# Performance work log

Hardware: AMD Instinct MI355X
Metric: run time of the kernel (lower is better)

Reference implementation:

```python
import jax, jax.numpy as jnp
import numpy as np

NEG = -1e30  # stands in for -inf on the diagonal; exp(NEG - max) == 0 exactly


def setup_inputs() -> dict:
    key = jax.random.key(0)
    k1, k2, k3, k4, k5 = jax.random.split(key, 5)
    B, C, H, W = 4, 512, 128, 128
    mid = C // 8  # 64
    x = jax.random.normal(k1, (B, C, H, W), dtype=jnp.float32)
    Wq = jax.random.normal(k2, (mid, C), dtype=jnp.float32) * (1.0 / np.sqrt(C))
    Wk = jax.random.normal(k3, (mid, C), dtype=jnp.float32) * (1.0 / np.sqrt(C))
    Wv = jax.random.normal(k4, (C, C), dtype=jnp.float32) * (1.0 / np.sqrt(C))
    gamma = jax.random.normal(k5, (1,), dtype=jnp.float32) * 0.1
    return {"x": x, "Wq": Wq, "Wk": Wk, "Wv": Wv, "gamma": gamma}


def reference(x, Wq, Wk, Wv, gamma):
    B, C, H, W = x.shape
    # 1x1 convs == channel matmuls
    q = jnp.einsum('bchw,mc->bmhw', x, Wq)  # (B, mid, H, W)
    k = jnp.einsum('bchw,mc->bmhw', x, Wk)
    v = jnp.einsum('bchw,dc->bdhw', x, Wv)  # (B, C, H, W)

    # vertical (H-axis) logits with -inf diagonal: eH[b,i,w,j] = sum_m q[b,m,i,w] k[b,m,j,w]
    eH = jnp.einsum('bmiw,bmjw->biwj', q, k)           # (B, H, W, H)
    diag = jnp.eye(H, dtype=bool)[:, None, :]          # (H, 1, H)
    eH = jnp.where(diag, NEG, eH)

    # horizontal (W-axis) logits: eW[b,h,i,j] = sum_m q[b,m,h,i] k[b,m,h,j]
    eW = jnp.einsum('bmhi,bmhj->bhij', q, k)           # (B, H, W, W)

    # joint softmax over the concatenated H+W logits
    attn = jax.nn.softmax(jnp.concatenate([eH, eW], axis=3), axis=3)  # (B, H, W, H+W)
    aH = attn[:, :, :, :H]  # (B, H, W, H)
    aW = attn[:, :, :, H:]  # (B, H, W, W)

    # attention-weighted value aggregation along each axis
    outH = jnp.einsum('bcjw,biwj->bciw', v, aH)  # (B, C, H, W)
    outW = jnp.einsum('bchj,bhij->bchi', v, aW)  # (B, C, H, W)

    return gamma[0] * (outH + outW) + x
```

## Files before the change

kernel.cpp:

```cpp
#include <hip/hip_runtime.h>
#include <cstdint>
#include <cstddef>

#define NEGV (-1e30f)

constexpr int C_ = 512, H_ = 128, W_ = 128;
constexpr int P_ = 16384;

typedef short bf16x8 __attribute__((ext_vector_type(8)));
typedef float f32x4  __attribute__((ext_vector_type(4)));
#define MFMA16(a, b, c) __builtin_amdgcn_mfma_f32_16x16x32_bf16((a), (b), (c), 0, 0, 0)

__device__ inline unsigned short f2bf(float f) {
    union { float f; uint32_t i; } t; t.f = f;
    uint32_t r = t.i + 0x7FFFu + ((t.i >> 16) & 1u);
    return (unsigned short)(r >> 16);
}
__device__ inline float bf2f(unsigned short u) {
    union { uint32_t i; float f; } t; t.i = (uint32_t)u << 16; return t.f;
}

__global__ __launch_bounds__(256) void kwconv(
    const float* __restrict__ Wq, const float* __restrict__ Wk,
    const float* __restrict__ Wv,
    unsigned short* __restrict__ Wqkbf, unsigned short* __restrict__ Wvbf)
{
    const int i4 = (blockIdx.x * 256 + threadIdx.x) * 4;
    const float* src; unsigned short* dst; int off;
    if (i4 < 32768)       { src = Wq + i4;          dst = Wqkbf + i4; }
    else if (i4 < 65536)  { off = i4 - 32768; src = Wk + off; dst = Wqkbf + i4; }
    else                  { off = i4 - 65536; src = Wv + off; dst = Wvbf + off; }
    const float4 v = *(const float4*)src;
    ushort4 u; u.x = f2bf(v.x); u.y = f2bf(v.y); u.z = f2bf(v.z); u.w = f2bf(v.w);
    *(ushort4*)dst = u;
}

__global__ __launch_bounds__(256) void kprep1(
    const float* __restrict__ x, unsigned short* __restrict__ xTbf)
{
    __shared__ float t[32][33];
    const int tx = threadIdx.x, ty = threadIdx.y;
    const int h0 = (blockIdx.x >> 2) * 32, w0 = (blockIdx.x & 3) * 32;
    const size_t base = (size_t)blockIdx.y * P_;
#pragma unroll
    for (int k = 0; k < 4; k++)
        t[ty + 8 * k][tx] = x[base + (size_t)(h0 + ty + 8 * k) * 128 + w0 + tx];
    __syncthreads();
#pragma unroll
    for (int k = 0; k < 4; k++)
        xTbf[base + (size_t)(w0 + ty + 8 * k) * 128 + h0 + tx] = f2bf(t[tx][ty + 8 * k]);
}

__global__ __launch_bounds__(256) void kprep2(
    const float* __restrict__ x, unsigned short* __restrict__ xbfT)
{
    __shared__ float t[32][33];
    const int tx = threadIdx.x, ty = threadIdx.y;
    const int p0 = blockIdx.x * 32, c0 = blockIdx.y * 32, b = blockIdx.z;
#pragma unroll
    for (int k = 0; k < 4; k++)
        t[ty + 8 * k][tx] = x[((size_t)(b * C_ + c0 + ty + 8 * k)) * P_ + p0 + tx];
    __syncthreads();
#pragma unroll
    for (int k = 0; k < 4; k++)
        xbfT[((size_t)b * P_ + p0 + ty + 8 * k) * C_ + c0 + tx] = f2bf(t[tx][ty + 8 * k]);
}

__global__ __launch_bounds__(256) void kgemm_mfma(
    const unsigned short* __restrict__ A, const unsigned short* __restrict__ Bm,
    unsigned short* __restrict__ outbf, float* __restrict__ outf,
    const float* __restrict__ addx, const float* __restrict__ gammap)
{
    __shared__ __attribute__((aligned(16))) unsigned short sA[128 * 72];
    __shared__ __attribute__((aligned(16))) unsigned short sB[128 * 72];
    const int tid = threadIdx.x;
    const int pbase = blockIdx.x * 128, mt = blockIdx.y, b = blockIdx.z;
    const int lane = tid & 63, wv = tid >> 6;
    const int m0 = (wv >> 1) * 64, p0 = (wv & 1) * 64;
    const int fr = lane & 15, fq = lane >> 4;

    f32x4 acc[4][4];
#pragma unroll
    for (int i = 0; i < 4; i++)
#pragma unroll
        for (int j = 0; j < 4; j++) acc[i][j] = (f32x4){0.f, 0.f, 0.f, 0.f};

    const size_t arow0 = (size_t)(mt * 128) * 512;
    const size_t brow0 = ((size_t)b * P_ + pbase) * 512;

    for (int kc = 0; kc < 512; kc += 64) {
#pragma unroll
        for (int rep = 0; rep < 4; rep++) {
            const int idx = rep * 256 + tid;
            const int kg = idx & 7, r = idx >> 3;
            *(uint4*)&sA[r * 72 + kg * 8] = *(const uint4*)&A[arow0 + (size_t)r * 512 + kc + kg * 8];
            *(uint4*)&sB[r * 72 + kg * 8] = *(const uint4*)&Bm[brow0 + (size_t)r * 512 + kc + kg * 8];
        }
        __syncthreads();
#pragma unroll
        for (int kk = 0; kk < 64; kk += 32) {
            bf16x8 af[4], bfv[4];
#pragma unroll
            for (int t = 0; t < 4; t++) af[t]  = *(const bf16x8*)&sA[(m0 + t * 16 + fr) * 72 + kk + fq * 8];
#pragma unroll
            for (int t = 0; t < 4; t++) bfv[t] = *(const bf16x8*)&sB[(p0 + t * 16 + fr) * 72 + kk + fq * 8];
#pragma unroll
            for (int i = 0; i < 4; i++)
#pragma unroll
                for (int j = 0; j < 4; j++)
                    acc[i][j] = MFMA16(af[i], bfv[j], acc[i][j]);
        }
        __syncthreads();
    }

    if (outbf) {
#pragma unroll
        for (int tj = 0; tj < 4; tj++) {
            const int p_g = pbase + p0 + tj * 16 + fr;
            const size_t rowo = ((size_t)b * P_ + p_g) * 128;
#pragma unroll
            for (int ti = 0; ti < 4; ti++) {
                const int mk = m0 + ti * 16 + fq * 4;
                ushort4 u;
                u.x = f2bf(acc[ti][tj][0]); u.y = f2bf(acc[ti][tj][1]);
                u.z = f2bf(acc[ti][tj][2]); u.w = f2bf(acc[ti][tj][3]);
                *(ushort4*)&outbf[rowo + mk] = u;
            }
        }
    } else {
        const float g = gammap[0];
#pragma unroll
        for (int ti = 0; ti < 4; ti++)
#pragma unroll
            for (int r = 0; r < 4; r++) {
                const int m_g = mt * 128 + m0 + ti * 16 + fq * 4 + r;
                const size_t rowo = ((size_t)(b * 512 + m_g)) * P_;
#pragma unroll
                for (int tj = 0; tj < 4; tj++) {
                    const int p_g = pbase + p0 + tj * 16 + fr;
                    outf[rowo + p_g] = fmaf(g, acc[ti][tj][r], addx[rowo + p_g]);
                }
            }
    }
}

__global__ __launch_bounds__(256) void klogits(
    const unsigned short* __restrict__ qkP, float* __restrict__ E,
    int rowMul, int rowStep, int mask)
{
    __shared__ __attribute__((aligned(16))) unsigned short sPM[128 * 136];
    const int tid = threadIdx.x;
    const int s = blockIdx.x, b = blockIdx.y;
    const size_t qbase = (size_t)b * P_ * 128;
    const int rb = s * rowMul;
#pragma unroll
    for (int rep = 0; rep < 8; rep++) {
        const int idx = rep * 256 + tid;
        const int mkg = idx & 15, i = idx >> 4;
        *(uint4*)&sPM[i * 136 + mkg * 8] =
            *(const uint4*)&qkP[qbase + (size_t)(rb + i * rowStep) * 128 + mkg * 8];
    }
    __syncthreads();

    const int lane = tid & 63, wv = tid >> 6;
    const int i0 = (wv >> 1) * 64, j0 = (wv & 1) * 64;
    const int fr = lane & 15, fq = lane >> 4;

    f32x4 acc[4][4];
#pragma unroll
    for (int i = 0; i < 4; i++)
#pragma unroll
        for (int j = 0; j < 4; j++) acc[i][j] = (f32x4){0.f, 0.f, 0.f, 0.f};

#pragma unroll
    for (int kk = 0; kk < 64; kk += 32) {
        bf16x8 af[4], bfv[4];
#pragma unroll
        for (int t = 0; t < 4; t++) af[t]  = *(const bf16x8*)&sPM[(i0 + t * 16 + fr) * 136 + kk + fq * 8];
#pragma unroll
        for (int t = 0; t < 4; t++) bfv[t] = *(const bf16x8*)&sPM[(j0 + t * 16 + fr) * 136 + 64 + kk + fq * 8];
#pragma unroll
        for (int i = 0; i < 4; i++)
#pragma unroll
            for (int j = 0; j < 4; j++)
                acc[i][j] = MFMA16(af[i], bfv[j], acc[i][j]);
    }

    float* Eb = E + ((size_t)(b * 128 + s)) * P_;
#pragma unroll
    for (int ti = 0; ti < 4; ti++)
#pragma unroll
        for (int r = 0; r < 4; r++) {
            const int i_g = i0 + ti * 16 + fq * 4 + r;
#pragma unroll
            for (int tj = 0; tj < 4; tj++) {
                const int j_g = j0 + tj * 16 + fr;
                float v = acc[ti][tj][r];
                if (mask && i_g == j_g) v = NEGV;
                Eb[(size_t)i_g * 128 + j_g] = v;
            }
        }
}

__global__ __launch_bounds__(256) void ksoftmax(
    const float* __restrict__ ER, const float* __restrict__ EC,
    unsigned short* __restrict__ AR, unsigned short* __restrict__ AC)
{
    const int lane = threadIdx.x & 63;
    const int pix = blockIdx.x * 4 + (threadIdx.x >> 6);
    const int b = pix >> 14, rem = pix & 16383;
    const int h = rem >> 7, w = rem & 127;
    const size_t ro = ((size_t)((b * 128 + h) * 128 + w)) * 128;
    const size_t co = ((size_t)((b * 128 + w) * 128 + h)) * 128;
    const float2 r = *(const float2*)(ER + ro + lane * 2);
    const float2 c = *(const float2*)(EC + co + lane * 2);
    float mx = fmaxf(fmaxf(r.x, r.y), fmaxf(c.x, c.y));
#pragma unroll
    for (int off = 32; off > 0; off >>= 1) mx = fmaxf(mx, __shfl_xor(mx, off));
    const float e0 = __expf(r.x - mx), e1 = __expf(r.y - mx);
    const float e2 = __expf(c.x - mx), e3 = __expf(c.y - mx);
    float sm = e0 + e1 + e2 + e3;
#pragma unroll
    for (int off = 32; off > 0; off >>= 1) sm += __shfl_xor(sm, off);
    const float inv = 1.0f / sm;
    ushort2 u0; u0.x = f2bf(e0 * inv); u0.y = f2bf(e1 * inv);
    ushort2 u1; u1.x = f2bf(e2 * inv); u1.y = f2bf(e3 * inv);
    *(ushort2*)(AR + ro + lane * 2) = u0;
    *(ushort2*)(AC + co + lane * 2) = u1;
}

__global__ __launch_bounds__(256) void kagg(
    const unsigned short* __restrict__ At, const float* __restrict__ Xf,
    const unsigned short* __restrict__ Xbf, unsigned short* __restrict__ ySumT,
    int pMul, int pStep, int rmw)
{
    __shared__ __attribute__((aligned(16))) unsigned short sA[128 * 72];
    __shared__ __attribute__((aligned(16))) unsigned short sB[128 * 72];
    const int tid = threadIdx.x;
    const int s = blockIdx.x, b = blockIdx.y, ct = blockIdx.z;
    const int lane = tid & 63, wv = tid >> 6;
    const int m0 = (wv >> 1) * 64, n0 = (wv & 1) * 64;
    const int fr = lane & 15, fq = lane >> 4;
    const size_t abase = ((size_t)(b * 128 + s)) * P_;

    f32x4 acc[4][4];
#pragma unroll
    for (int i = 0; i < 4; i++)
#pragma unroll
        for (int j = 0; j < 4; j++) acc[i][j] = (f32x4){0.f, 0.f, 0.f, 0.f};

    for (int kc = 0; kc < 128; kc += 64) {
#pragma unroll
        for (int rep = 0; rep < 4; rep++) {
            const int idx = rep * 256 + tid;
            const int jg = idx & 7, i = idx >> 3;
            *(uint4*)&sA[i * 72 + jg * 8] = *(const uint4*)&At[abase + (size_t)i * 128 + kc + jg * 8];
        }
        if (Xf) {
#pragma unroll
            for (int rep = 0; rep < 8; rep++) {
                const int idx = rep * 256 + tid;
                const int jq = idx & 15, cc = idx >> 4;
                const float4 v = *(const float4*)&Xf[((size_t)(b * C_ + ct * 128 + cc)) * P_ + s * 128 + kc + jq * 4];
                ushort4 u; u.x = f2bf(v.x); u.y = f2bf(v.y); u.z = f2bf(v.z); u.w = f2bf(v.w);
                *(ushort4*)&sB[cc * 72 + jq * 4] = u;
            }
        } else {
#pragma unroll
            for (int rep = 0; rep < 4; rep++) {
                const int idx = rep * 256 + tid;
                const int jg = idx & 7, cc = idx >> 3;
                *(uint4*)&sB[cc * 72 + jg * 8] =
                    *(const uint4*)&Xbf[((size_t)(b * C_ + ct * 128 + cc)) * P_ + s * 128 + kc + jg * 8];
            }
        }
        __syncthreads();
#pragma unroll
        for (int kk = 0; kk < 64; kk += 32) {
            bf16x8 af[4], bfv[4];
#pragma unroll
            for (int t = 0; t < 4; t++) af[t]  = *(const bf16x8*)&sA[(m0 + t * 16 + fr) * 72 + kk + fq * 8];
#pragma unroll
            for (int t = 0; t < 4; t++) bfv[t] = *(const bf16x8*)&sB[(n0 + t * 16 + fr) * 72 + kk + fq * 8];
#pragma unroll
            for (int i = 0; i < 4; i++)
#pragma unroll
                for (int j = 0; j < 4; j++)
                    acc[i][j] = MFMA16(af[i], bfv[j], acc[i][j]);
        }
        __syncthreads();
    }

#pragma unroll
    for (int ti = 0; ti < 4; ti++)
#pragma unroll
        for (int r = 0; r < 4; r++) {
            const int i_g = m0 + ti * 16 + fq * 4 + r;
            const size_t p = (size_t)s * pMul + (size_t)i_g * pStep;
            const size_t rowo = ((size_t)b * P_ + p) * 512;
#pragma unroll
            for (int tc = 0; tc < 4; tc++) {
                const int c_g = ct * 128 + n0 + tc * 16 + fr;
                float v = acc[ti][tc][r];
                if (rmw) v += bf2f(ySumT[rowo + c_g]);
                ySumT[rowo + c_g] = f2bf(v);
            }
        }
}

extern "C" void kernel_launch(void* const* d_in, const int* in_sizes, int n_in,
                              void* d_out, int out_size, void* d_ws, size_t ws_size,
                              hipStream_t stream) {
    const float* x     = (const float*)d_in[0];
    const float* Wq    = (const float*)d_in[1];
    const float* Wk    = (const float*)d_in[2];
    const float* Wv    = (const float*)d_in[3];
    const float* gamma = (const float*)d_in[4];
    float* out = (float*)d_out;

    char* base = (char*)d_ws;
    unsigned short* Wqkbf = (unsigned short*)base;             base += 131072;
    unsigned short* Wvbf  = (unsigned short*)base;             base += 524288;
    unsigned short* xTbf  = (unsigned short*)base;             base += 67108864;
    unsigned short* xbfT  = (unsigned short*)base;             base += 67108864;
    unsigned short* qkP   = (unsigned short*)base;             base += 16777216;
    float*          ERow  = (float*)base;                      base += 33554432;
    float*          ECol  = (float*)base;                      base += 33554432;
    unsigned short* ARow  = (unsigned short*)base;             base += 16777216;
    unsigned short* ACol  = (unsigned short*)base;             base += 16777216;
    unsigned short* ySumT = (unsigned short*)base;             base += 67108864;

    kwconv<<<320, 256, 0, stream>>>(Wq, Wk, Wv, Wqkbf, Wvbf);
    kprep1<<<dim3(16, 2048), dim3(32, 8), 0, stream>>>(x, xTbf);
    kprep2<<<dim3(512, 16, 4), dim3(32, 8), 0, stream>>>(x, xbfT);
    kgemm_mfma<<<dim3(128, 1, 4), 256, 0, stream>>>(Wqkbf, xbfT, qkP, nullptr, nullptr, nullptr);
    klogits<<<dim3(128, 4), 256, 0, stream>>>(qkP, ERow, 128, 1, 0);
    klogits<<<dim3(128, 4), 256, 0, stream>>>(qkP, ECol, 1, 128, 1);
    ksoftmax<<<16384, 256, 0, stream>>>(ERow, ECol, ARow, ACol);
    kagg<<<dim3(128, 4, 4), 256, 0, stream>>>(ARow, x, nullptr, ySumT, 128, 1, 0);
    kagg<<<dim3(128, 4, 4), 256, 0, stream>>>(ACol, nullptr, xTbf, ySumT, 1, 128, 1);
    kgemm_mfma<<<dim3(128, 4, 4), 256, 0, stream>>>(Wvbf, ySumT, nullptr, out, x, gamma);
}
```

Measured before the change: 553.8 us.

## Merge aggregation passes into one kernel with separate row/column sums and swizzled LDS

Replaces the two kagg launches, which read-modify-write a shared ySumT buffer, with one kagg2 launch. It writes row and column aggregates to separate buffers, the column one aliasing the no-longer-needed ERow, and loops over all four channel tiles while keeping the attention tile resident in swizzled LDS. The final value GEMM sums the two bf16 buffers while loading its B operand. The two logits launches are also merged via blockIdx.z. This removes the RMW read pass and the repeated attention loads, at the cost of extra bf16 adds and rounding in the final GEMM's load path and a larger LDS footprint per block.

New measurement: 558.4 us. No clear change (+0.8%).

```diff
diff --git a/kernel.cpp b/kernel.cpp
--- a/kernel.cpp
+++ b/kernel.cpp
@@ -10,6 +10,8 @@
 typedef short bf16x8 __attribute__((ext_vector_type(8)));
 typedef float f32x4  __attribute__((ext_vector_type(4)));
 #define MFMA16(a, b, c) __builtin_amdgcn_mfma_f32_16x16x32_bf16((a), (b), (c), 0, 0, 0)
+
+#define SWZI(r, cu) ((((r) << 7)) + (((((cu) >> 3) ^ ((r) & 15))) << 3) + ((cu) & 7))
 
 __device__ inline unsigned short f2bf(float f) {
     union { float f; uint32_t i; } t; t.f = f;
@@ -18,6 +20,17 @@
 }
 __device__ inline float bf2f(unsigned short u) {
     union { uint32_t i; float f; } t; t.i = (uint32_t)u << 16; return t.f;
+}
+__device__ inline uint32_t bfadd2(uint32_t a, uint32_t b) {
+    union { uint32_t i; float f; } alo, ahi, blo, bhi;
+    alo.i = a << 16; ahi.i = a & 0xffff0000u;
+    blo.i = b << 16; bhi.i = b & 0xffff0000u;
+    const float lo = alo.f + blo.f, hi = ahi.f + bhi.f;
+    return (uint32_t)f2bf(lo) | ((uint32_t)f2bf(hi) << 16);
+}
+__device__ inline uint4 bfadd8(const uint4 a, const uint4 b) {
+    uint4 r; r.x = bfadd2(a.x, b.x); r.y = bfadd2(a.y, b.y);
+    r.z = bfadd2(a.z, b.z); r.w = bfadd2(a.w, b.w); return r;
 }
 
 __global__ __launch_bounds__(256) void kwconv(
@@ -68,6 +81,7 @@
 
 __global__ __launch_bounds__(256) void kgemm_mfma(
     const unsigned short* __restrict__ A, const unsigned short* __restrict__ Bm,
+    const unsigned short* __restrict__ Bm2,
     unsigned short* __restrict__ outbf, float* __restrict__ outf,
     const float* __restrict__ addx, const float* __restrict__ gammap)
 {
@@ -94,7 +108,10 @@
             const int idx = rep * 256 + tid;
             const int kg = idx & 7, r = idx >> 3;
             *(uint4*)&sA[r * 72 + kg * 8] = *(const uint4*)&A[arow0 + (size_t)r * 512 + kc + kg * 8];
-            *(uint4*)&sB[r * 72 + kg * 8] = *(const uint4*)&Bm[brow0 + (size_t)r * 512 + kc + kg * 8];
+            const size_t boff = brow0 + (size_t)r * 512 + kc + kg * 8;
+            uint4 vb = *(const uint4*)&Bm[boff];
+            if (Bm2) vb = bfadd8(vb, *(const uint4*)&Bm2[boff]);
+            *(uint4*)&sB[r * 72 + kg * 8] = vb;
         }
         __syncthreads();
 #pragma unroll
@@ -145,12 +162,15 @@
 }
 
 __global__ __launch_bounds__(256) void klogits(
-    const unsigned short* __restrict__ qkP, float* __restrict__ E,
-    int rowMul, int rowStep, int mask)
+    const unsigned short* __restrict__ qkP,
+    float* __restrict__ ERow, float* __restrict__ ECol)
 {
     __shared__ __attribute__((aligned(16))) unsigned short sPM[128 * 136];
     const int tid = threadIdx.x;
-    const int s = blockIdx.x, b = blockIdx.y;
+    const int s = blockIdx.x, b = blockIdx.y, mode = blockIdx.z;
+    const int rowMul  = mode ? 1 : 128;
+    const int rowStep = mode ? 128 : 1;
+    float* E = mode ? ECol : ERow;
     const size_t qbase = (size_t)b * P_ * 128;
     const int rb = s * rowMul;
 #pragma unroll
@@ -196,7 +216,7 @@
             for (int tj = 0; tj < 4; tj++) {
                 const int j_g = j0 + tj * 16 + fr;
                 float v = acc[ti][tj][r];
-                if (mask && i_g == j_g) v = NEGV;
+                if (mode && i_g == j_g) v = NEGV;
                 Eb[(size_t)i_g * 128 + j_g] = v;
             }
         }
@@ -229,83 +249,86 @@
     *(ushort2*)(AC + co + lane * 2) = u1;
 }
 
-__global__ __launch_bounds__(256) void kagg(
-    const unsigned short* __restrict__ At, const float* __restrict__ Xf,
-    const unsigned short* __restrict__ Xbf, unsigned short* __restrict__ ySumT,
-    int pMul, int pStep, int rmw)
-{
-    __shared__ __attribute__((aligned(16))) unsigned short sA[128 * 72];
-    __shared__ __attribute__((aligned(16))) unsigned short sB[128 * 72];
+__global__ __launch_bounds__(256) void kagg2(
+    const unsigned short* __restrict__ ARow, const unsigned short* __restrict__ ACol,
+    const float* __restrict__ x, const unsigned short* __restrict__ xTbf,
+    unsigned short* __restrict__ ySumR, unsigned short* __restrict__ ySumC)
+{
+    __shared__ __attribute__((aligned(16))) unsigned short sAttn[128 * 128];
+    __shared__ __attribute__((aligned(16))) unsigned short sX[128 * 128];
     const int tid = threadIdx.x;
-    const int s = blockIdx.x, b = blockIdx.y, ct = blockIdx.z;
+    const int s = blockIdx.x, b = blockIdx.y, mode = blockIdx.z;
     const int lane = tid & 63, wv = tid >> 6;
     const int m0 = (wv >> 1) * 64, n0 = (wv & 1) * 64;
     const int fr = lane & 15, fq = lane >> 4;
-    const size_t abase = ((size_t)(b * 128 + s)) * P_;
-
-    f32x4 acc[4][4];
-#pragma unroll
-    for (int i = 0; i < 4; i++)
-#pragma unroll
-        for (int j = 0; j < 4; j++) acc[i][j] = (f32x4){0.f, 0.f, 0.f, 0.f};
-
-    for (int kc = 0; kc < 128; kc += 64) {
-#pragma unroll
-        for (int rep = 0; rep < 4; rep++) {
-            const int idx = rep * 256 + tid;
-            const int jg = idx & 7, i = idx >> 3;
-            *(uint4*)&sA[i * 72 + jg * 8] = *(const uint4*)&At[abase + (size_t)i * 128 + kc + jg * 8];
-        }
-        if (Xf) {
+
+    const unsigned short* At = (mode ? ACol : ARow) + ((size_t)(b * 128 + s)) * P_;
+#pragma unroll
+    for (int rep = 0; rep < 8; rep++) {
+        const int idx = rep * 256 + tid;
+        const int jg = idx & 15, row = idx >> 4;
+        *(uint4*)&sAttn[SWZI(row, jg * 8)] = *(const uint4*)&At[(size_t)row * 128 + jg * 8];
+    }
+
+    unsigned short* yS = mode ? ySumC : ySumR;
+
+    for (int ct = 0; ct < 4; ct++) {
+        if (mode == 0) {
+#pragma unroll
+            for (int rep = 0; rep < 16; rep++) {
+                const int idx = rep * 256 + tid;
+                const int jq = idx & 31, cc = idx >> 5;
+                const float4 v = *(const float4*)&x[((size_t)(b * C_ + ct * 128 + cc)) * P_ + s * 128 + jq * 4];
+                ushort4 u; u.x = f2bf(v.x); u.y = f2bf(v.y); u.z = f2bf(v.z); u.w = f2bf(v.w);
+                *(ushort4*)&sX[SWZI(cc, jq * 4)] = u;
+            }
+        } else {
 #pragma unroll
             for (int rep = 0; rep < 8; rep++) {
                 const int idx = rep * 256 + tid;
-                const int jq = idx & 15, cc = idx >> 4;
-                const float4 v = *(const float4*)&Xf[((size_t)(b * C_ + ct * 128 + cc)) * P_ + s * 128 + kc + jq * 4];
-                ushort4 u; u.x = f2bf(v.x); u.y = f2bf(v.y); u.z = f2bf(v.z); u.w = f2bf(v.w);
-                *(ushort4*)&sB[cc * 72 + jq * 4] = u;
-            }
-        } else {
-#pragma unroll
-            for (int rep = 0; rep < 4; rep++) {
-                const int idx = rep * 256 + tid;
-                const int jg = idx & 7, cc = idx >> 3;
-                *(uint4*)&sB[cc * 72 + jg * 8] =
-                    *(const uint4*)&Xbf[((size_t)(b * C_ + ct * 128 + cc)) * P_ + s * 128 + kc + jg * 8];
+                const int jg = idx & 15, cc = idx >> 4;
+                *(uint4*)&sX[SWZI(cc, jg * 8)] =
+                    *(const uint4*)&xTbf[((size_t)(b * C_ + ct * 128 + cc)) * P_ + s * 128 + jg * 8];
             }
         }
         __syncthreads();
-#pragma unroll
-        for (int kk = 0; kk < 64; kk += 32) {
+
+        f32x4 acc[4][4];
+#pragma unroll
+        for (int i = 0; i < 4; i++)
+#pragma unroll
+            for (int j = 0; j < 4; j++) acc[i][j] = (f32x4){0.f, 0.f, 0.f, 0.f};
+
+#pragma unroll
+        for (int kk = 0; kk < 128; kk += 32) {
             bf16x8 af[4], bfv[4];
 #pragma unroll
-            for (int t = 0; t < 4; t++) af[t]  = *(const bf16x8*)&sA[(m0 + t * 16 + fr) * 72 + kk + fq * 8];
-#pragma unroll
-            for (int t = 0; t < 4; t++) bfv[t] = *(const bf16x8*)&sB[(n0 + t * 16 + fr) * 72 + kk + fq * 8];
+            for (int t = 0; t < 4; t++) af[t]  = *(const bf16x8*)&sX[SWZI(m0 + t * 16 + fr, kk + fq * 8)];
+#pragma unroll
+            for (int t = 0; t < 4; t++) bfv[t] = *(const bf16x8*)&sAttn[SWZI(n0 + t * 16 + fr, kk + fq * 8)];
 #pragma unroll
             for (int i = 0; i < 4; i++)
 #pragma unroll
                 for (int j = 0; j < 4; j++)
                     acc[i][j] = MFMA16(af[i], bfv[j], acc[i][j]);
         }
+
+        const int cg0 = ct * 128 + m0 + fq * 4;
+#pragma unroll
+        for (int tj = 0; tj < 4; tj++) {
+            const int i_g = n0 + tj * 16 + fr;
+            const size_t p = mode ? ((size_t)i_g * 128 + s) : ((size_t)s * 128 + i_g);
+            unsigned short* rowp = yS + ((size_t)b * P_ + p) * 512;
+#pragma unroll
+            for (int ti = 0; ti < 4; ti++) {
+                ushort4 u;
+                u.x = f2bf(acc[ti][tj][0]); u.y = f2bf(acc[ti][tj][1]);
+                u.z = f2bf(acc[ti][tj][2]); u.w = f2bf(acc[ti][tj][3]);
+                *(ushort4*)&rowp[cg0 + ti * 16] = u;
+            }
+        }
         __syncthreads();
     }
-
-#pragma unroll
-    for (int ti = 0; ti < 4; ti++)
-#pragma unroll
-        for (int r = 0; r < 4; r++) {
-            const int i_g = m0 + ti * 16 + fq * 4 + r;
-            const size_t p = (size_t)s * pMul + (size_t)i_g * pStep;
-            const size_t rowo = ((size_t)b * P_ + p) * 512;
-#pragma unroll
-            for (int tc = 0; tc < 4; tc++) {
-                const int c_g = ct * 128 + n0 + tc * 16 + fr;
-                float v = acc[ti][tc][r];
-                if (rmw) v += bf2f(ySumT[rowo + c_g]);
-                ySumT[rowo + c_g] = f2bf(v);
-            }
-        }
 }
 
 extern "C" void kernel_launch(void* const* d_in, const int* in_sizes, int n_in,
@@ -328,16 +351,15 @@
     float*          ECol  = (float*)base;                      base += 33554432;
     unsigned short* ARow  = (unsigned short*)base;             base += 16777216;
     unsigned short* ACol  = (unsigned short*)base;             base += 16777216;
-    unsigned short* ySumT = (unsigned short*)base;             base += 67108864;
+    unsigned short* ySumR = (unsigned short*)base;             base += 67108864;
+    unsigned short* ySumC = (unsigned short*)ERow;
 
     kwconv<<<320, 256, 0, stream>>>(Wq, Wk, Wv, Wqkbf, Wvbf);
     kprep1<<<dim3(16, 2048), dim3(32, 8), 0, stream>>>(x, xTbf);
     kprep2<<<dim3(512, 16, 4), dim3(32, 8), 0, stream>>>(x, xbfT);
-    kgemm_mfma<<<dim3(128, 1, 4), 256, 0, stream>>>(Wqkbf, xbfT, qkP, nullptr, nullptr, nullptr);
-    klogits<<<dim3(128, 4), 256, 0, stream>>>(qkP, ERow, 128, 1, 0);
-    klogits<<<dim3(128, 4), 256, 0, stream>>>(qkP, ECol, 1, 128, 1);
+    kgemm_mfma<<<dim3(128, 1, 4), 256, 0, stream>>>(Wqkbf, xbfT, nullptr, qkP, nullptr, nullptr, nullptr);
+    klogits<<<dim3(128, 4, 2), 256, 0, stream>>>(qkP, ERow, ECol);
     ksoftmax<<<16384, 256, 0, stream>>>(ERow, ECol, ARow, ACol);
-    kagg<<<dim3(128, 4, 4), 256, 0, stream>>>(ARow, x, nullptr, ySumT, 128, 1, 0);
-    kagg<<<dim3(128, 4, 4), 256, 0, stream>>>(ACol, nullptr, xTbf, ySumT, 1, 128, 1);
-    kgemm_mfma<<<dim3(128, 4, 4), 256, 0, stream>>>(Wvbf, ySumT, nullptr, out, x, gamma);
-}
+    kagg2<<<dim3(128, 4, 2), 256, 0, stream>>>(ARow, ACol, x, xTbf, ySumR, ySumC);
+    kgemm_mfma<<<dim3(128, 4, 4), 256, 0, stream>>>(Wvbf, ySumR, ySumC, nullptr, out, x, gamma);
+}
```
